# Optimization experiments

Hardware: AMD Instinct MI355X
Metric: run time of the kernel (lower is better)

Reference implementation:

```python
import jax, jax.numpy as jnp
import numpy as np

BLOCK = 256      # fixed sequence length (causal mask size)
N_EMBD = 384
N_HEAD = 6
HEAD = N_EMBD // N_HEAD  # 64
LN_EPS = 1e-5
B = 512


def setup_inputs() -> dict:
    key = jax.random.key(0)
    k0, k1, k2 = jax.random.split(key, 3)
    logits = jax.random.normal(k0, (B, BLOCK, N_EMBD), dtype=jnp.float32)
    ln_gamma = jnp.ones((N_EMBD,), jnp.float32)
    ln_beta = jnp.zeros((N_EMBD,), jnp.float32)
    # per-head fused QKV weight: (H, E, 3*HEAD), bias-free like nn.Linear(N_EMBD, 3*HEAD, bias=False)
    w_qkv = jax.random.normal(k1, (N_HEAD, N_EMBD, 3 * HEAD), dtype=jnp.float32) * 0.02
    w_proj = jax.random.normal(k2, (N_EMBD, N_EMBD), dtype=jnp.float32) * 0.02
    b_proj = jnp.zeros((N_EMBD,), jnp.float32)
    return {"logits": logits, "ln_gamma": ln_gamma, "ln_beta": ln_beta,
            "w_qkv": w_qkv, "w_proj": w_proj, "b_proj": b_proj}


def reference(logits, ln_gamma, ln_beta, w_qkv, w_proj, b_proj):
    # LayerNorm over last dim (applied BEFORE attention, as in the torch module)
    mu = jnp.mean(logits, axis=-1, keepdims=True)
    var = jnp.mean(jnp.square(logits - mu), axis=-1, keepdims=True)
    x = (logits - mu) * jax.lax.rsqrt(var + LN_EPS) * ln_gamma + ln_beta

    # fused per-head QKV projection: (B,S,E) x (H,E,3d) -> (B,H,S,3d)
    qkv = jnp.einsum('bse,hed->bhsd', x, w_qkv)
    q, k, v = jnp.split(qkv, 3, axis=-1)  # each (B,H,S,HEAD)

    scale = HEAD ** -0.5
    scores = jnp.einsum('bhqd,bhkd->bhqk', q, k) * scale  # (B,H,S,S)
    causal = jnp.tril(jnp.ones((BLOCK, BLOCK), dtype=bool))
    scores = jnp.where(causal, scores, -jnp.inf)
    attn = jax.nn.softmax(scores, axis=-1)

    out = jnp.einsum('bhqk,bhkd->bhqd', attn, v)          # (B,H,S,HEAD)
    out = out.transpose(0, 2, 1, 3).reshape(B, BLOCK, N_EMBD)  # concat heads
    return out @ w_proj + b_proj
```

## Files before the change

### kernel.cpp

```cpp
#include <hip/hip_runtime.h>

typedef __attribute__((ext_vector_type(8))) short bf16x8;
typedef __attribute__((ext_vector_type(4))) float f32x4;
typedef __attribute__((ext_vector_type(4))) unsigned int u32x4;
typedef unsigned short u16;
typedef unsigned int u32;

__device__ __forceinline__ u16 f2bf(float f) {
    union { float f; u32 u; } c; c.f = f;
    return (u16)((c.u + 0x7FFFu + ((c.u >> 16) & 1u)) >> 16);
}

__device__ __forceinline__ u16 f2bf_rna(float f) {
    union { float f; u32 u; } c; c.f = f;
    return (u16)((c.u + 0x8000u) >> 16);
}

__device__ __forceinline__ bf16x8 ld16(const void* p) {
    union { uint4 u; bf16x8 v; } c;
    c.u = *reinterpret_cast<const uint4*>(p);
    return c.v;
}

__global__ void prep_kernel(const float* __restrict__ wqkv, const float* __restrict__ wproj,
                            u16* __restrict__ Wqt, u16* __restrict__ Wpt) {
    int idx = blockIdx.x * 256 + threadIdx.x;
    if (idx < 6 * 192 * 384) {
        int k = idx % 384;
        int n = idx / 384;
        int h = n / 192, dd = n % 192;
        Wqt[idx] = f2bf(wqkv[(h * 384 + k) * 192 + dd]);
    }
    if (idx < 384 * 384) {
        int k = idx % 384, n = idx / 384;
        Wpt[idx] = f2bf(wproj[k * 384 + n]);
    }
}

__global__ __launch_bounds__(256) void ln_kernel(const float* __restrict__ x,
                                                 const float* __restrict__ gamma,
                                                 const float* __restrict__ beta,
                                                 u16* __restrict__ xln) {
    int row = blockIdx.x * 4 + (threadIdx.x >> 6);
    int l = threadIdx.x & 63;
    const float* xr = x + (size_t)row * 384;
    float2 v[3];
    float s = 0.f, sq = 0.f;
#pragma unroll
    for (int i = 0; i < 3; ++i) {
        v[i] = *reinterpret_cast<const float2*>(xr + i * 128 + l * 2);
        s += v[i].x + v[i].y;
        sq += v[i].x * v[i].x + v[i].y * v[i].y;
    }
#pragma unroll
    for (int m = 1; m < 64; m <<= 1) {
        s += __shfl_xor(s, m, 64);
        sq += __shfl_xor(sq, m, 64);
    }
    float mean = s * (1.0f / 384.0f);
    float var = sq * (1.0f / 384.0f) - mean * mean;
    float rstd = rsqrtf(var + 1e-5f);
#pragma unroll
    for (int i = 0; i < 3; ++i) {
        int c = i * 128 + l * 2;
        float y0 = (v[i].x - mean) * rstd * gamma[c] + beta[c];
        float y1 = (v[i].y - mean) * rstd * gamma[c + 1] + beta[c + 1];
        u32 packed = (u32)f2bf(y0) | ((u32)f2bf(y1) << 16);
        *reinterpret_cast<u32*>(xln + (size_t)row * 384 + c) = packed;
    }
}

__global__ __launch_bounds__(256, 2) void qkv_kernel(const u16* __restrict__ xln,
                                                     const u16* __restrict__ Wqt,
                                                     u16* __restrict__ qkvout) {
    __shared__ u16 S[40960];
    u16* Asb[2] = {S, S + 8192};
    u16* Bsb[2] = {S + 16384, S + 28672};
    const int mt = blockIdx.x;
    const int h = blockIdx.y;
    const int t = threadIdx.x;
    const int l = t & 63, w = t >> 6;
    const int wm = w >> 1, wn = w & 1;
    const int l15 = l & 15, lq = l >> 4;
    const int rloc = l >> 3, seg = l & 7;
    const int m0 = mt * 128;
    const u16* Ag = xln + (size_t)m0 * 384;
    const u16* Bg = Wqt + (size_t)h * 192 * 384;
    f32x4 acc[4][6];
#pragma unroll
    for (int rg = 0; rg < 4; ++rg)
#pragma unroll
        for (int cg = 0; cg < 6; ++cg) acc[rg][cg] = (f32x4){0.f, 0.f, 0.f, 0.f};

    auto stage = [&](int kt, int buf) {
#pragma unroll
        for (int i = 0; i < 4; ++i) {
            int row = w * 32 + i * 8 + rloc;
            int ss = seg ^ (row & 7);
            __builtin_amdgcn_global_load_lds(Ag + (size_t)row * 384 + kt * 64 + ss * 8,
                                             &Asb[buf][(w * 32 + i * 8) * 64], 16, 0, 0);
        }
#pragma unroll
        for (int i = 0; i < 6; ++i) {
            int row = w * 48 + i * 8 + rloc;
            int ss = seg ^ (row & 7);
            __builtin_amdgcn_global_load_lds(Bg + (size_t)row * 384 + kt * 64 + ss * 8,
                                             &Bsb[buf][(w * 48 + i * 8) * 64], 16, 0, 0);
        }
    };

    stage(0, 0);
    __syncthreads();

    for (int kt = 0; kt < 6; ++kt) {
        const int cur = kt & 1;
        if (kt < 5) stage(kt + 1, cur ^ 1);
        char* Ab = reinterpret_cast<char*>(Asb[cur]);
        char* Bb = reinterpret_cast<char*>(Bsb[cur]);
        bf16x8 af[4][2], bf[6][2];
#pragma unroll
        for (int rg = 0; rg < 4; ++rg)
#pragma unroll
            for (int kk = 0; kk < 2; ++kk) {
                int row = wm * 64 + rg * 16 + l15;
                af[rg][kk] = ld16(Ab + row * 128 + ((kk * 64 + lq * 16) ^ ((row & 7) << 4)));
            }
#pragma unroll
        for (int cg = 0; cg < 6; ++cg)
#pragma unroll
            for (int kk = 0; kk < 2; ++kk) {
                int row = wn * 96 + cg * 16 + l15;
                bf[cg][kk] = ld16(Bb + row * 128 + ((kk * 64 + lq * 16) ^ ((row & 7) << 4)));
            }
#pragma unroll
        for (int kk = 0; kk < 2; ++kk)
#pragma unroll
            for (int rg = 0; rg < 4; ++rg)
#pragma unroll
                for (int cg = 0; cg < 6; ++cg)
                    acc[rg][cg] = __builtin_amdgcn_mfma_f32_16x16x32_bf16(af[rg][kk], bf[cg][kk], acc[rg][cg], 0, 0, 0);
        __syncthreads();
    }
    u16* tile = S;
#pragma unroll
    for (int rg = 0; rg < 4; ++rg)
#pragma unroll
        for (int cg = 0; cg < 6; ++cg)
#pragma unroll
            for (int r = 0; r < 4; ++r) {
                int s_loc = wm * 64 + rg * 16 + lq * 4 + r;
                int dd = wn * 96 + cg * 16 + l15;
                tile[s_loc * 192 + dd] = f2bf(acc[rg][cg][r]);
            }
    __syncthreads();
    const int b = m0 >> 8;
    const int s0 = m0 & 255;
    u16* outp = qkvout + ((size_t)(b * 6 + h) * 256 + s0) * 192;
#pragma unroll
    for (int i = 0; i < 12; ++i) {
        int idx = t + 256 * i;
        u32x4 v = *reinterpret_cast<const u32x4*>(tile + idx * 8);
        __builtin_nontemporal_store(v, reinterpret_cast<u32x4*>(outp + idx * 8));
    }
}

__global__ __launch_bounds__(512, 2) void attn_kernel(const u16* __restrict__ qkv,
                                                      u16* __restrict__ aout) {
    __shared__ u16 Ks[256 * 64];
    __shared__ u16 Vt[64 * 256];
    __shared__ u16 Ps[8 * 16 * 64];
    const int bh = blockIdx.x;
    const int b = bh / 6, h = bh % 6;
    const u16* base = qkv + (size_t)bh * (256 * 192);
    const int t = threadIdx.x;
    const int w = t >> 6, l = t & 63;
    const int l15 = l & 15, lq = l >> 4;

#pragma unroll
    for (int i = 0; i < 4; ++i) {
        int u = t + 512 * i;
        int row = u >> 3, seg = u & 7;
        uint4 v = *reinterpret_cast<const uint4*>(base + row * 192 + 64 + seg * 8);
        *reinterpret_cast<uint4*>(reinterpret_cast<char*>(Ks) + row * 128 + ((seg * 16) ^ ((row & 7) << 4))) = v;
    }
    {
        int j = t >> 1, d0 = (t & 1) * 32;
#pragma unroll
        for (int c = 0; c < 4; ++c) {
            uint4 v = *reinterpret_cast<const uint4*>(base + j * 192 + 128 + d0 + c * 8);
            const u16* pv = reinterpret_cast<const u16*>(&v);
#pragma unroll
            for (int e = 0; e < 8; ++e) {
                int d = d0 + c * 8 + e;
                *reinterpret_cast<u16*>(reinterpret_cast<char*>(Vt) + d * 512 + ((j * 2) ^ ((d & 7) << 4))) = pv[e];
            }
        }
    }
    const int qrow0 = w * 16;
    const int qrow1 = (15 - w) * 16;
    const int kbmax0 = w >> 2;
    const int kbmax1 = (15 - w) >> 2;
    bf16x8 qf[2][2];
#pragma unroll
    for (int kk = 0; kk < 2; ++kk) {
        qf[0][kk] = ld16(base + (qrow0 + l15) * 192 + kk * 32 + lq * 8);
        qf[1][kk] = ld16(base + (qrow1 + l15) * 192 + kk * 32 + lq * 8);
    }
    __syncthreads();

    f32x4 acc[2][4];
#pragma unroll
    for (int rg = 0; rg < 2; ++rg)
#pragma unroll
        for (int dg = 0; dg < 4; ++dg) acc[rg][dg] = (f32x4){0.f, 0.f, 0.f, 0.f};
    float m_r[2][4], l_r[2][4];
#pragma unroll
    for (int rg = 0; rg < 2; ++rg)
#pragma unroll
        for (int r = 0; r < 4; ++r) { m_r[rg][r] = -3.0e38f; l_r[rg][r] = 0.f; }

    const float CEXP = 0.18033688011112042f;
    char* pbase = reinterpret_cast<char*>(Ps) + w * 2048;

    for (int kb = 0; kb <= kbmax1; ++kb) {
        const bool do0 = (kb <= kbmax0);
        f32x4 sc[2][4];
#pragma unroll
        for (int rg = 0; rg < 2; ++rg)
#pragma unroll
            for (int cg = 0; cg < 4; ++cg) sc[rg][cg] = (f32x4){0.f, 0.f, 0.f, 0.f};
#pragma unroll
        for (int kk = 0; kk < 2; ++kk) {
            bf16x8 kf[4];
#pragma unroll
            for (int cg = 0; cg < 4; ++cg) {
                int krow = kb * 64 + cg * 16 + l15;
                kf[cg] = ld16(reinterpret_cast<char*>(Ks) + krow * 128 + ((kk * 64 + lq * 16) ^ ((krow & 7) << 4)));
            }
            if (do0)
#pragma unroll
                for (int cg = 0; cg < 4; ++cg)
                    sc[0][cg] = __builtin_amdgcn_mfma_f32_16x16x32_bf16(qf[0][kk], kf[cg], sc[0][cg], 0, 0, 0);
#pragma unroll
            for (int cg = 0; cg < 4; ++cg)
                sc[1][cg] = __builtin_amdgcn_mfma_f32_16x16x32_bf16(qf[1][kk], kf[cg], sc[1][cg], 0, 0, 0);
        }
#pragma unroll
        for (int rg = 0; rg < 2; ++rg) {
            if (rg == 0 && !do0) continue;
            const int qb = rg ? qrow1 : qrow0;
            const int diag = rg ? kbmax1 : kbmax0;
            if (kb == diag) {
#pragma unroll
                for (int cg = 0; cg < 4; ++cg)
#pragma unroll
                    for (int r = 0; r < 4; ++r) {
                        int gq = qb + lq * 4 + r;
                        int gk = kb * 64 + cg * 16 + l15;
                        if (gk > gq) sc[rg][cg][r] = -3.0e38f;
                    }
            }
            float fac[4], rs[4];
#pragma unroll
            for (int r = 0; r < 4; ++r) {
                float mx = fmaxf(fmaxf(sc[rg][0][r], sc[rg][1][r]), fmaxf(sc[rg][2][r], sc[rg][3][r]));
#pragma unroll
                for (int s = 1; s < 16; s <<= 1) mx = fmaxf(mx, __shfl_xor(mx, s, 64));
                float mn = fmaxf(m_r[rg][r], mx);
                fac[r] = exp2f((m_r[rg][r] - mn) * CEXP);
                m_r[rg][r] = mn;
                rs[r] = 0.f;
            }
#pragma unroll
            for (int cg = 0; cg < 4; ++cg)
#pragma unroll
                for (int r = 0; r < 4; ++r) {
                    float p = exp2f((sc[rg][cg][r] - m_r[rg][r]) * CEXP);
                    sc[rg][cg][r] = p;
                    rs[r] += p;
                }
#pragma unroll
            for (int r = 0; r < 4; ++r) {
#pragma unroll
                for (int s = 1; s < 16; s <<= 1) rs[r] += __shfl_xor(rs[r], s, 64);
                l_r[rg][r] = l_r[rg][r] * fac[r] + rs[r];
            }
#pragma unroll
            for (int dg = 0; dg < 4; ++dg)
#pragma unroll
                for (int r = 0; r < 4; ++r) acc[rg][dg][r] *= fac[r];
#pragma unroll
            for (int cg = 0; cg < 4; ++cg)
#pragma unroll
                for (int r = 0; r < 4; ++r) {
                    int row = lq * 4 + r;
                    int col = cg * 16 + l15;
                    *reinterpret_cast<u16*>(pbase + row * 128 + ((col * 2) ^ ((row & 7) << 4))) = f2bf_rna(sc[rg][cg][r]);
                }
#pragma unroll
            for (int kk = 0; kk < 2; ++kk) {
                bf16x8 vf[4];
#pragma unroll
                for (int dg = 0; dg < 4; ++dg) {
                    int d = dg * 16 + l15;
                    vf[dg] = ld16(reinterpret_cast<char*>(Vt) + d * 512 + ((kb * 128 + kk * 64 + lq * 16) ^ ((d & 7) << 4)));
                }
                bf16x8 pf = ld16(pbase + l15 * 128 + ((kk * 64 + lq * 16) ^ ((l15 & 7) << 4)));
#pragma unroll
                for (int dg = 0; dg < 4; ++dg)
                    acc[rg][dg] = __builtin_amdgcn_mfma_f32_16x16x32_bf16(pf, vf[dg], acc[rg][dg], 0, 0, 0);
            }
        }
    }
#pragma unroll
    for (int rg = 0; rg < 2; ++rg) {
        const int qb = rg ? qrow1 : qrow0;
#pragma unroll
        for (int r = 0; r < 4; ++r) {
            float inv = 1.0f / l_r[rg][r];
            int gq = qb + lq * 4 + r;
            u16* orow = aout + ((size_t)b * 256 + gq) * 384 + h * 64;
#pragma unroll
            for (int dg = 0; dg < 4; ++dg) orow[dg * 16 + l15] = f2bf(acc[rg][dg][r] * inv);
        }
    }
}

__global__ __launch_bounds__(256, 2) void proj_kernel(const u16* __restrict__ A,
                                                      const u16* __restrict__ Wpt,
                                                      const float* __restrict__ bias,
                                                      float* __restrict__ out) {
    __shared__ u16 S[32768];
    u16* Asb[2] = {S, S + 8192};
    u16* Bsb[2] = {S + 16384, S + 24576};
    const int mt = blockIdx.x;
    const int nt = blockIdx.y;
    const int t = threadIdx.x;
    const int l = t & 63, w = t >> 6;
    const int wm = w >> 1, wn = w & 1;
    const int l15 = l & 15, lq = l >> 4;
    const int rloc = l >> 3, seg = l & 7;
    const int m0 = mt * 128;
    const u16* Ag = A + (size_t)m0 * 384;
    const u16* Bg = Wpt + (size_t)nt * 128 * 384;
    f32x4 acc[4][4];
#pragma unroll
    for (int rg = 0; rg < 4; ++rg)
#pragma unroll
        for (int cg = 0; cg < 4; ++cg) acc[rg][cg] = (f32x4){0.f, 0.f, 0.f, 0.f};

    auto stage = [&](int kt, int buf) {
#pragma unroll
        for (int i = 0; i < 4; ++i) {
            int row = w * 32 + i * 8 + rloc;
            int ss = seg ^ (row & 7);
            __builtin_amdgcn_global_load_lds(Ag + (size_t)row * 384 + kt * 64 + ss * 8,
                                             &Asb[buf][(w * 32 + i * 8) * 64], 16, 0, 0);
            __builtin_amdgcn_global_load_lds(Bg + (size_t)row * 384 + kt * 64 + ss * 8,
                                             &Bsb[buf][(w * 32 + i * 8) * 64], 16, 0, 0);
        }
    };

    stage(0, 0);
    __syncthreads();

    for (int kt = 0; kt < 6; ++kt) {
        const int cur = kt & 1;
        if (kt < 5) stage(kt + 1, cur ^ 1);
        char* Ab = reinterpret_cast<char*>(Asb[cur]);
        char* Bb = reinterpret_cast<char*>(Bsb[cur]);
        bf16x8 af[4][2], bf[4][2];
#pragma unroll
        for (int rg = 0; rg < 4; ++rg)
#pragma unroll
            for (int kk = 0; kk < 2; ++kk) {
                int row = wm * 64 + rg * 16 + l15;
                af[rg][kk] = ld16(Ab + row * 128 + ((kk * 64 + lq * 16) ^ ((row & 7) << 4)));
            }
#pragma unroll
        for (int cg = 0; cg < 4; ++cg)
#pragma unroll
            for (int kk = 0; kk < 2; ++kk) {
                int row = wn * 64 + cg * 16 + l15;
                bf[cg][kk] = ld16(Bb + row * 128 + ((kk * 64 + lq * 16) ^ ((row & 7) << 4)));
            }
#pragma unroll
        for (int kk = 0; kk < 2; ++kk)
#pragma unroll
            for (int rg = 0; rg < 4; ++rg)
#pragma unroll
                for (int cg = 0; cg < 4; ++cg)
                    acc[rg][cg] = __builtin_amdgcn_mfma_f32_16x16x32_bf16(af[rg][kk], bf[cg][kk], acc[rg][cg], 0, 0, 0);
        __syncthreads();
    }
    float* ftile = reinterpret_cast<float*>(S);
#pragma unroll
    for (int rg = 0; rg < 4; ++rg)
#pragma unroll
        for (int cg = 0; cg < 4; ++cg) {
            int n_loc = wn * 64 + cg * 16 + l15;
            float bv = bias[nt * 128 + n_loc];
#pragma unroll
            for (int r = 0; r < 4; ++r) {
                int m_loc = wm * 64 + rg * 16 + lq * 4 + r;
                ftile[m_loc * 128 + n_loc] = acc[rg][cg][r] + bv;
            }
        }
    __syncthreads();
    float* outp = out + (size_t)m0 * 384 + nt * 128;
#pragma unroll
    for (int i = 0; i < 16; ++i) {
        int idx = t + 256 * i;
        int row = idx >> 5;
        int c = (idx & 31) * 4;
        u32x4 v = *reinterpret_cast<const u32x4*>(ftile + row * 128 + c);
        __builtin_nontemporal_store(v, reinterpret_cast<u32x4*>(outp + (size_t)row * 384 + c));
    }
}

extern "C" void kernel_launch(void* const* d_in, const int* in_sizes, int n_in,
                              void* d_out, int out_size, void* d_ws, size_t ws_size,
                              hipStream_t stream) {
    const float* logits = (const float*)d_in[0];
    const float* gamma  = (const float*)d_in[1];
    const float* beta   = (const float*)d_in[2];
    const float* wqkv   = (const float*)d_in[3];
    const float* wproj  = (const float*)d_in[4];
    const float* bproj  = (const float*)d_in[5];
    float* out = (float*)d_out;

    char* ws = (char*)d_ws;
    u16* Wqt  = (u16*)(ws);
    u16* Wpt  = (u16*)(ws + 884736);
    u16* xln  = (u16*)(ws + 1179648);
    u16* qkvb = (u16*)(ws + 101842944);
    u16* attnout = xln;

    hipLaunchKernelGGL(prep_kernel, dim3(1728), dim3(256), 0, stream, wqkv, wproj, Wqt, Wpt);
    hipLaunchKernelGGL(ln_kernel, dim3(32768), dim3(256), 0, stream, logits, gamma, beta, xln);
    hipLaunchKernelGGL(qkv_kernel, dim3(1024, 6), dim3(256), 0, stream, xln, Wqt, qkvb);
    hipLaunchKernelGGL(attn_kernel, dim3(3072), dim3(512), 0, stream, qkvb, attnout);
    hipLaunchKernelGGL(proj_kernel, dim3(1024, 3), dim3(256), 0, stream, attnout, Wpt, bproj, out);
}
```

Before: 478.9 us.

## Shrink QKV GEMM K-tile to 32 and raise occupancy, store output directly

The QKV projection kernel now stages K in chunks of 32 instead of 64, which halves the LDS footprint and shortens the per-iteration fragment arrays. Launch bounds go from 2 to 3 blocks per CU to raise occupancy. The LDS-staged, coalesced nontemporal output write is replaced by direct scattered 2-byte global stores from accumulators. The risks are twice as many barriers per tile and a much less coalesced output store pattern.

```diff
diff --git a/kernel.cpp b/kernel.cpp
--- a/kernel.cpp
+++ b/kernel.cpp
@@ -70,19 +70,19 @@
     }
 }
 
-__global__ __launch_bounds__(256, 2) void qkv_kernel(const u16* __restrict__ xln,
+__global__ __launch_bounds__(256, 3) void qkv_kernel(const u16* __restrict__ xln,
                                                      const u16* __restrict__ Wqt,
                                                      u16* __restrict__ qkvout) {
-    __shared__ u16 S[40960];
-    u16* Asb[2] = {S, S + 8192};
-    u16* Bsb[2] = {S + 16384, S + 28672};
+    __shared__ u16 As[2][128 * 32];
+    __shared__ u16 Bs[2][192 * 32];
     const int mt = blockIdx.x;
     const int h = blockIdx.y;
     const int t = threadIdx.x;
     const int l = t & 63, w = t >> 6;
     const int wm = w >> 1, wn = w & 1;
     const int l15 = l & 15, lq = l >> 4;
-    const int rloc = l >> 3, seg = l & 7;
+    const int rloc = l >> 2;
+    const int ss = (l & 3) ^ ((l >> 2) & 3);
     const int m0 = mt * 128;
     const u16* Ag = xln + (size_t)m0 * 384;
     const u16* Bg = Wqt + (size_t)h * 192 * 384;
@@ -94,74 +94,58 @@
 
     auto stage = [&](int kt, int buf) {
 #pragma unroll
-        for (int i = 0; i < 4; ++i) {
-            int row = w * 32 + i * 8 + rloc;
-            int ss = seg ^ (row & 7);
-            __builtin_amdgcn_global_load_lds(Ag + (size_t)row * 384 + kt * 64 + ss * 8,
-                                             &Asb[buf][(w * 32 + i * 8) * 64], 16, 0, 0);
-        }
-#pragma unroll
-        for (int i = 0; i < 6; ++i) {
-            int row = w * 48 + i * 8 + rloc;
-            int ss = seg ^ (row & 7);
-            __builtin_amdgcn_global_load_lds(Bg + (size_t)row * 384 + kt * 64 + ss * 8,
-                                             &Bsb[buf][(w * 48 + i * 8) * 64], 16, 0, 0);
+        for (int i = 0; i < 2; ++i) {
+            int row = w * 32 + i * 16 + rloc;
+            __builtin_amdgcn_global_load_lds(Ag + (size_t)row * 384 + kt * 32 + ss * 8,
+                                             &As[buf][(w * 32 + i * 16) * 32], 16, 0, 0);
+        }
+#pragma unroll
+        for (int i = 0; i < 3; ++i) {
+            int row = w * 48 + i * 16 + rloc;
+            __builtin_amdgcn_global_load_lds(Bg + (size_t)row * 384 + kt * 32 + ss * 8,
+                                             &Bs[buf][(w * 48 + i * 16) * 32], 16, 0, 0);
         }
     };
 
     stage(0, 0);
     __syncthreads();
 
-    for (int kt = 0; kt < 6; ++kt) {
+    for (int kt = 0; kt < 12; ++kt) {
         const int cur = kt & 1;
-        if (kt < 5) stage(kt + 1, cur ^ 1);
-        char* Ab = reinterpret_cast<char*>(Asb[cur]);
-        char* Bb = reinterpret_cast<char*>(Bsb[cur]);
-        bf16x8 af[4][2], bf[6][2];
+        if (kt < 11) stage(kt + 1, cur ^ 1);
+        char* Ab = reinterpret_cast<char*>(As[cur]);
+        char* Bb = reinterpret_cast<char*>(Bs[cur]);
+        bf16x8 af[4], bf[6];
+#pragma unroll
+        for (int rg = 0; rg < 4; ++rg) {
+            int row = wm * 64 + rg * 16 + l15;
+            af[rg] = ld16(Ab + row * 64 + ((lq * 16) ^ ((row & 3) << 4)));
+        }
+#pragma unroll
+        for (int cg = 0; cg < 6; ++cg) {
+            int row = wn * 96 + cg * 16 + l15;
+            bf[cg] = ld16(Bb + row * 64 + ((lq * 16) ^ ((row & 3) << 4)));
+        }
 #pragma unroll
         for (int rg = 0; rg < 4; ++rg)
 #pragma unroll
-            for (int kk = 0; kk < 2; ++kk) {
-                int row = wm * 64 + rg * 16 + l15;
-                af[rg][kk] = ld16(Ab + row * 128 + ((kk * 64 + lq * 16) ^ ((row & 7) << 4)));
-            }
-#pragma unroll
-        for (int cg = 0; cg < 6; ++cg)
-#pragma unroll
-            for (int kk = 0; kk < 2; ++kk) {
-                int row = wn * 96 + cg * 16 + l15;
-                bf[cg][kk] = ld16(Bb + row * 128 + ((kk * 64 + lq * 16) ^ ((row & 7) << 4)));
-            }
-#pragma unroll
-        for (int kk = 0; kk < 2; ++kk)
-#pragma unroll
-            for (int rg = 0; rg < 4; ++rg)
-#pragma unroll
-                for (int cg = 0; cg < 6; ++cg)
-                    acc[rg][cg] = __builtin_amdgcn_mfma_f32_16x16x32_bf16(af[rg][kk], bf[cg][kk], acc[rg][cg], 0, 0, 0);
+            for (int cg = 0; cg < 6; ++cg)
+                acc[rg][cg] = __builtin_amdgcn_mfma_f32_16x16x32_bf16(af[rg], bf[cg], acc[rg][cg], 0, 0, 0);
         __syncthreads();
     }
-    u16* tile = S;
-#pragma unroll
-    for (int rg = 0; rg < 4; ++rg)
-#pragma unroll
-        for (int cg = 0; cg < 6; ++cg)
-#pragma unroll
-            for (int r = 0; r < 4; ++r) {
-                int s_loc = wm * 64 + rg * 16 + lq * 4 + r;
-                int dd = wn * 96 + cg * 16 + l15;
-                tile[s_loc * 192 + dd] = f2bf(acc[rg][cg][r]);
-            }
-    __syncthreads();
     const int b = m0 >> 8;
     const int s0 = m0 & 255;
-    u16* outp = qkvout + ((size_t)(b * 6 + h) * 256 + s0) * 192;
-#pragma unroll
-    for (int i = 0; i < 12; ++i) {
-        int idx = t + 256 * i;
-        u32x4 v = *reinterpret_cast<const u32x4*>(tile + idx * 8);
-        __builtin_nontemporal_store(v, reinterpret_cast<u32x4*>(outp + idx * 8));
-    }
+    u16* out = qkvout + ((size_t)(b * 6 + h) * 256) * 192;
+#pragma unroll
+    for (int rg = 0; rg < 4; ++rg)
+#pragma unroll
+        for (int cg = 0; cg < 6; ++cg)
+#pragma unroll
+            for (int r = 0; r < 4; ++r) {
+                int s = s0 + wm * 64 + rg * 16 + lq * 4 + r;
+                int dd = wn * 96 + cg * 16 + l15;
+                out[(size_t)s * 192 + dd] = f2bf(acc[rg][cg][r]);
+            }
 }
 
 __global__ __launch_bounds__(512, 2) void attn_kernel(const u16* __restrict__ qkv,
```

Measured after the change: 464.8 us. -2.9%, faster.
